# Optimization experiments

Hardware: AMD Instinct MI355X
Metric: run time of the kernel (lower is better)

## Reference

```python
import jax, jax.numpy as jnp
import numpy as np

K = 10
SLOPE = 0.2
FEATS = [3, 64, 128, 256, 512, 1024]
MLP = [1024, 128, 64, 1]
B, N = 8, 2048


def setup_inputs() -> dict:
    key = jax.random.key(0)
    keys = jax.random.split(key, 32)
    inp = {"x": jax.random.normal(keys[0], (B, N, 3), dtype=jnp.float32)}
    ki = 1
    for i in range(5):
        fin, fout = 2 * FEATS[i], FEATS[i + 1]
        s = 1.0 / np.sqrt(fin)
        inp[f"w{i}"] = jax.random.uniform(keys[ki], (fin, fout), jnp.float32, -s, s); ki += 1
        inp[f"b{i}"] = jax.random.uniform(keys[ki], (fout,), jnp.float32, -s, s); ki += 1
    for i in range(3):
        fin, fout = MLP[i], MLP[i + 1]
        s = 1.0 / np.sqrt(fin)
        inp[f"m{i}w"] = jax.random.uniform(keys[ki], (fin, fout), jnp.float32, -s, s); ki += 1
        inp[f"m{i}b"] = jax.random.uniform(keys[ki], (fout,), jnp.float32, -s, s); ki += 1
    return inp


def _knn_idx(xb):
    # xb: [N, F]; squared euclidean distances, self included (dist 0)
    sq = jnp.sum(xb * xb, axis=-1)
    d2 = sq[:, None] + sq[None, :] - 2.0 * (xb @ xb.T)
    _, idx = jax.lax.top_k(-d2, K)  # [N, K] nearest (incl. self)
    return idx


def _edge_conv(x, W, b):
    # x: [B, N, F] -> [B, N, Fout]
    fin = x.shape[-1]
    W1, W2 = W[:fin], W[fin:]  # split concat([x_i, x_j - x_i]) @ W
    idx = jax.vmap(_knn_idx)(x)  # [B, N, K]
    x_j = jax.vmap(lambda xb, ib: xb[ib])(x, idx)  # [B, N, K, F]
    h_center = x @ W1 + b  # [B, N, Fout]
    diff = x_j - x[:, :, None, :]
    h = h_center[:, :, None, :] + jnp.einsum('bnkf,fo->bnko', diff, W2)
    h = jnp.where(h > 0, h, SLOPE * h)  # LeakyReLU(0.2)
    return jnp.max(h, axis=2)  # max aggregation over neighbors


def reference(x, w0, b0, w1, b1, w2, b2, w3, b3, w4, b4,
              m0w, m0b, m1w, m1b, m2w, m2b):
    ws = [(w0, b0), (w1, b1), (w2, b2), (w3, b3), (w4, b4)]
    h = x
    for W, b in ws:
        h = _edge_conv(h, W, b)
    g = jnp.max(h, axis=1)  # MaxPool1d(kernel=2048) -> global max over points: [B, 1024]
    g = g @ m0w + m0b
    g = g @ m1w + m1b
    g = g @ m2w + m2b
    return g  # [B, 1]
```

## Files before the change

kernel.cpp:

```cpp
#include <hip/hip_runtime.h>
#include <hip/hip_bf16.h>
#include <math.h>

#define BB 8
#define NN 2048
#define KK 10
#define BN (BB * NN)
#define HC 1024
#define GCH 64

typedef __attribute__((ext_vector_type(8))) short bf16x8;
typedef __attribute__((ext_vector_type(4))) float f32x4;

__device__ inline unsigned short f2bf(float f) {
    unsigned int u = __float_as_uint(f);
    unsigned int r = u + 0x7fffu + ((u >> 16) & 1u);
    return (unsigned short)(r >> 16);
}
__device__ inline float bf2f(unsigned short h) {
    return __uint_as_float((unsigned int)h << 16);
}

__device__ __forceinline__ void async16(const void* g, void* l) {
    __builtin_amdgcn_global_load_lds(
        (const __attribute__((address_space(1))) void*)g,
        (__attribute__((address_space(3))) void*)l, 16, 0, 0);
}

__global__ void xsplit3_kernel(const float* __restrict__ x,
                               unsigned short* __restrict__ hi,
                               unsigned short* __restrict__ lo,
                               float* __restrict__ sq) {
    int row = blockIdx.x * blockDim.x + threadIdx.x;
    if (row >= BN) return;
    unsigned short hbuf[32], lbuf[32];
#pragma unroll
    for (int f = 0; f < 32; ++f) { hbuf[f] = 0; lbuf[f] = 0; }
    float s = 0.f;
#pragma unroll
    for (int f = 0; f < 3; ++f) {
        float v = x[(size_t)row * 3 + f];
        s += v * v;
        unsigned short h = f2bf(v);
        hbuf[f] = h;
        lbuf[f] = f2bf(v - bf2f(h));
    }
    sq[row] = s;
#pragma unroll
    for (int f = 0; f < 32; f += 8) {
        *(uint4*)&hi[(size_t)row * 32 + f] = *(uint4*)&hbuf[f];
        *(uint4*)&lo[(size_t)row * 32 + f] = *(uint4*)&lbuf[f];
    }
}

__global__ __launch_bounds__(256) void knn_gram_kernel(
        const unsigned short* __restrict__ xh, const unsigned short* __restrict__ xl,
        const float* __restrict__ sq, float* __restrict__ d2a,
        float* __restrict__ d2b, int F) {
    int b = blockIdx.y;
    int t = blockIdx.x, ti = 0;
    while (t >= 16 - ti) { t -= 16 - ti; ti++; }
    int tj = ti + t;
    int row0 = ti * 128;
    int col0 = tj * 128;
    const unsigned short* xhb = xh + (size_t)b * NN * F;
    const unsigned short* xlb = xl + (size_t)b * NN * F;
    const float* sqb = sq + (size_t)b * NN;

    __shared__ __align__(16) unsigned char smem_raw[33024];
    unsigned short* Ah = (unsigned short*)smem_raw;
    unsigned short* Al = Ah + 128 * 32;
    unsigned short* Bh = Al + 128 * 32;
    unsigned short* Bl = Bh + 128 * 32;
    float* LT = (float*)smem_raw;

    int tid = threadIdx.x;
    int lane = tid & 63;
    int wave = tid >> 6;
    int wr = (wave >> 1) * 64, wc = (wave & 1) * 64;
    int l15 = lane & 15, kq = lane >> 4;
    int rsub = lane >> 2;
    int csub = (((lane & 3) ^ ((lane >> 3) & 3))) * 8;
    int kqs = (kq ^ ((l15 >> 1) & 3)) * 8;

    f32x4 acc[4][4];
#pragma unroll
    for (int mt = 0; mt < 4; ++mt)
#pragma unroll
        for (int nt = 0; nt < 4; ++nt) acc[mt][nt] = (f32x4){0.f, 0.f, 0.f, 0.f};

    for (int kc = 0; kc < F; kc += 32) {
        __syncthreads();
#pragma unroll
        for (int j = 0; j < 2; ++j) {
            int row = wave * 32 + j * 16 + rsub;
            int dsto = wave * 1024 + j * 512;
            async16(xhb + (size_t)(row0 + row) * F + kc + csub, Ah + dsto);
            async16(xlb + (size_t)(row0 + row) * F + kc + csub, Al + dsto);
            async16(xhb + (size_t)(col0 + row) * F + kc + csub, Bh + dsto);
            async16(xlb + (size_t)(col0 + row) * F + kc + csub, Bl + dsto);
        }
        __syncthreads();
        bf16x8 bh[4], bl[4];
#pragma unroll
        for (int t4 = 0; t4 < 4; ++t4) {
            bh[t4] = *(const bf16x8*)&Bh[(wc + t4 * 16 + l15) * 32 + kqs];
            bl[t4] = *(const bf16x8*)&Bl[(wc + t4 * 16 + l15) * 32 + kqs];
        }
#pragma unroll
        for (int mt = 0; mt < 4; ++mt) {
            bf16x8 ah = *(const bf16x8*)&Ah[(wr + mt * 16 + l15) * 32 + kqs];
            bf16x8 al = *(const bf16x8*)&Al[(wr + mt * 16 + l15) * 32 + kqs];
#pragma unroll
            for (int nt = 0; nt < 4; ++nt) {
                acc[mt][nt] = __builtin_amdgcn_mfma_f32_16x16x32_bf16(ah, bh[nt], acc[mt][nt], 0, 0, 0);
                acc[mt][nt] = __builtin_amdgcn_mfma_f32_16x16x32_bf16(al, bh[nt], acc[mt][nt], 0, 0, 0);
                acc[mt][nt] = __builtin_amdgcn_mfma_f32_16x16x32_bf16(ah, bl[nt], acc[mt][nt], 0, 0, 0);
            }
        }
    }
    {
        float* dst = (col0 < HC) ? d2a : d2b;
        int lc0 = col0 & (HC - 1);
#pragma unroll
        for (int mt = 0; mt < 4; ++mt) {
            int rbase = row0 + wr + mt * 16 + kq * 4;
#pragma unroll
            for (int nt = 0; nt < 4; ++nt) {
                int cc = wc + nt * 16 + l15;
                float sqc = sqb[col0 + cc];
#pragma unroll
                for (int r = 0; r < 4; ++r) {
                    float v = (sqb[rbase + r] + sqc) - 2.f * acc[mt][nt][r];
                    acc[mt][nt][r] = v;
                    dst[((size_t)b * NN + rbase + r) * HC + lc0 + cc] = v;
                }
            }
        }
    }
    if (ti != tj) {
        float* mdst = (row0 < HC) ? d2a : d2b;
        int mc0 = row0 & (HC - 1);
#pragma unroll
        for (int h = 0; h < 2; ++h) {
            __syncthreads();
            if ((wave & 1) == h) {
#pragma unroll
                for (int mt = 0; mt < 4; ++mt)
#pragma unroll
                    for (int nt = 0; nt < 4; ++nt)
#pragma unroll
                        for (int r = 0; r < 4; ++r)
                            LT[(nt * 16 + l15) * 129 + (wr + mt * 16 + kq * 4 + r)] =
                                acc[mt][nt][r];
            }
            __syncthreads();
#pragma unroll
            for (int it = 0; it < 8; ++it) {
                int v = tid + it * 256;
                int lr = v >> 5, c4 = v & 31;
                float4 val;
                val.x = LT[lr * 129 + c4 * 4];
                val.y = LT[lr * 129 + c4 * 4 + 1];
                val.z = LT[lr * 129 + c4 * 4 + 2];
                val.w = LT[lr * 129 + c4 * 4 + 3];
                *(float4*)&mdst[((size_t)b * NN + col0 + h * 64 + lr) * HC + mc0 + c4 * 4] = val;
            }
        }
    }
}

__global__ __launch_bounds__(256) void knn_select_kernel(
        const float* __restrict__ d2a, const float* __restrict__ d2b,
        int* __restrict__ idx) {
    int row = blockIdx.x * 4 + (threadIdx.x >> 6);
    int lane = threadIdx.x & 63;
    const float* ra = d2a + (size_t)row * HC;
    const float* rb = d2b + (size_t)row * HC;

    float4 v[8];
#pragma unroll
    for (int it = 0; it < 4; ++it) {
        v[it]     = *(const float4*)&ra[it * 256 + lane * 4];
        v[it + 4] = *(const float4*)&rb[it * 256 + lane * 4];
    }

    float bestd[KK];
    int besti[KK];
#pragma unroll
    for (int k = 0; k < KK; ++k) { bestd[k] = INFINITY; besti[k] = 0x7fffffff; }

#pragma unroll
    for (int it = 0; it < 8; ++it) {
        int cbase = ((it < 4) ? (it * 256) : (HC + (it - 4) * 256)) + lane * 4;
        float dv[4] = {v[it].x, v[it].y, v[it].z, v[it].w};
#pragma unroll
        for (int s4 = 0; s4 < 4; ++s4) {
            float d = dv[s4];
            if (d < bestd[KK - 1]) {
                bestd[KK - 1] = d;
                besti[KK - 1] = cbase + s4;
#pragma unroll
                for (int s = KK - 1; s > 0; --s) {
                    if (bestd[s] < bestd[s - 1]) {
                        float td = bestd[s]; bestd[s] = bestd[s - 1]; bestd[s - 1] = td;
                        int ti = besti[s]; besti[s] = besti[s - 1]; besti[s - 1] = ti;
                    }
                }
            }
        }
    }

    int h = 0;
    int mywin = 0;
    for (int s = 0; s < KK; ++s) {
        float dd = (h < KK) ? bestd[h] : INFINITY;
        int ii = (h < KK) ? besti[h] : 0x7fffffff;
        float d0 = dd; int i0 = ii;
#pragma unroll
        for (int off = 32; off > 0; off >>= 1) {
            float od = __shfl_xor(dd, off);
            int oi = __shfl_xor(ii, off);
            if (od < dd || (od == dd && oi < ii)) { dd = od; ii = oi; }
        }
        if (lane == s) mywin = ii;
        if (h < KK && i0 == ii && d0 == dd) h++;
    }
    if (lane < KK) idx[(size_t)row * KK + lane] = mywin;
}

__global__ void wsplit_kernel(const float* __restrict__ w, unsigned short* __restrict__ WT,
                              int fin, int fpad, int fout) {
    int i = blockIdx.x * blockDim.x + threadIdx.x;
    int total = 2 * fout * fpad;
    if (i >= total) return;
    int op = i % (2 * fout);
    int f = i / (2 * fout);
    float v = 0.f;
    if (f < fin) {
        if (op < fout) v = w[(size_t)f * fout + op] - w[(size_t)(fin + f) * fout + op];
        else v = w[(size_t)(fin + f) * fout + (op - fout)];
    }
    unsigned short h = f2bf(v);
    unsigned short l = f2bf(v - bf2f(h));
    WT[(size_t)op * (2 * fpad) + f] = h;
    WT[(size_t)op * (2 * fpad) + fpad + f] = l;
}

__global__ __launch_bounds__(256) void gemm2_mfma_kernel(
        const unsigned short* __restrict__ XSh, const unsigned short* __restrict__ XSl,
        const unsigned short* __restrict__ WT, const float* __restrict__ bias,
        float* __restrict__ Aout, float* __restrict__ Tout, int fin, int fout) {
    int m0 = blockIdx.x * 128;
    int n0 = blockIdx.y * 128;
    __shared__ __align__(16) unsigned short AsB[4 * 128 * 32];
    unsigned short* Ah = AsB;
    unsigned short* Al = Ah + 128 * 32;
    unsigned short* Bh = Al + 128 * 32;
    unsigned short* Bl = Bh + 128 * 32;

    int tid = threadIdx.x;
    int lane = tid & 63;
    int wave = tid >> 6;
    int wr = (wave >> 1) * 64, wc = (wave & 1) * 64;
    int l15 = lane & 15, kq = lane >> 4;
    int rsub = lane >> 2;
    int csub = (((lane & 3) ^ ((lane >> 3) & 3))) * 8;
    int kqs = (kq ^ ((l15 >> 1) & 3)) * 8;
    int w2f = 2 * fin;

    f32x4 acc[4][4];
#pragma unroll
    for (int mt = 0; mt < 4; ++mt)
#pragma unroll
        for (int nt = 0; nt < 4; ++nt) acc[mt][nt] = (f32x4){0.f, 0.f, 0.f, 0.f};

    for (int kc = 0; kc < fin; kc += 32) {
        __syncthreads();
#pragma unroll
        for (int j = 0; j < 2; ++j) {
            int row = wave * 32 + j * 16 + rsub;
            int dsto = wave * 1024 + j * 512;
            async16(XSh + (size_t)(m0 + row) * fin + kc + csub, Ah + dsto);
            async16(XSl + (size_t)(m0 + row) * fin + kc + csub, Al + dsto);
            async16(WT + (size_t)(n0 + row) * w2f + kc + csub, Bh + dsto);
            async16(WT + (size_t)(n0 + row) * w2f + fin + kc + csub, Bl + dsto);
        }
        __syncthreads();
        bf16x8 bh[4], bl[4];
#pragma unroll
        for (int t = 0; t < 4; ++t) {
            bh[t] = *(const bf16x8*)&Bh[(wc + t * 16 + l15) * 32 + kqs];
            bl[t] = *(const bf16x8*)&Bl[(wc + t * 16 + l15) * 32 + kqs];
        }
#pragma unroll
        for (int mt = 0; mt < 4; ++mt) {
            bf16x8 ah = *(const bf16x8*)&Ah[(wr + mt * 16 + l15) * 32 + kqs];
            bf16x8 al = *(const bf16x8*)&Al[(wr + mt * 16 + l15) * 32 + kqs];
#pragma unroll
            for (int nt = 0; nt < 4; ++nt) {
                acc[mt][nt] = __builtin_amdgcn_mfma_f32_16x16x32_bf16(ah, bh[nt], acc[mt][nt], 0, 0, 0);
                acc[mt][nt] = __builtin_amdgcn_mfma_f32_16x16x32_bf16(al, bh[nt], acc[mt][nt], 0, 0, 0);
                acc[mt][nt] = __builtin_amdgcn_mfma_f32_16x16x32_bf16(ah, bl[nt], acc[mt][nt], 0, 0, 0);
            }
        }
    }
#pragma unroll
    for (int mt = 0; mt < 4; ++mt) {
        int mbase = m0 + wr + mt * 16 + kq * 4;
#pragma unroll
        for (int nt = 0; nt < 4; ++nt) {
            int oc = n0 + wc + nt * 16 + l15;
            f32x4 c = acc[mt][nt];
            if (oc < fout) {
                float bv = bias[oc];
#pragma unroll
                for (int r = 0; r < 4; ++r)
                    Aout[(size_t)(mbase + r) * fout + oc] = c[r] + bv;
            } else {
                int o2 = oc - fout;
#pragma unroll
                for (int r = 0; r < 4; ++r)
                    Tout[(size_t)(mbase + r) * fout + o2] = c[r];
            }
        }
    }
}

__global__ __launch_bounds__(256) void gathermax_fused_kernel(
        const float* __restrict__ A, const float* __restrict__ T,
        const int* __restrict__ idx, unsigned short* __restrict__ hi,
        unsigned short* __restrict__ lo, float* __restrict__ sq, int shift) {
    int b = blockIdx.y;
    int wave = threadIdx.x >> 6;
    int lane = threadIdx.x & 63;
    int pnl = blockIdx.x * 4 + wave;
    int pn = (b << 11) + pnl;
    int fout = 1 << shift;
    int nf4 = fout >> 2;
    const float* Tb = T + ((size_t)b << 11) * fout;
    const int* ip = idx + (size_t)pn * KK;
    int j[KK];
#pragma unroll
    for (int k = 0; k < KK; ++k) j[k] = ip[k];

    float s = 0.f;
    for (int f4 = lane; f4 < nf4; f4 += 64) {
        int o = f4 * 4;
        float4 m = {-INFINITY, -INFINITY, -INFINITY, -INFINITY};
#pragma unroll
        for (int k = 0; k < KK; ++k) {
            float4 t = *(const float4*)&Tb[(size_t)j[k] * fout + o];
            m.x = fmaxf(m.x, t.x); m.y = fmaxf(m.y, t.y);
            m.z = fmaxf(m.z, t.z); m.w = fmaxf(m.w, t.w);
        }
        float4 a = *(const float4*)&A[(size_t)pn * fout + o];
        float h4[4];
        h4[0] = a.x + m.x; h4[1] = a.y + m.y; h4[2] = a.z + m.z; h4[3] = a.w + m.w;
        uint2 uh, ul;
        unsigned short hs[4], ls[4];
#pragma unroll
        for (int q = 0; q < 4; ++q) {
            float h = h4[q] > 0.f ? h4[q] : 0.2f * h4[q];
            s += h * h;
            unsigned short hh = f2bf(h);
            hs[q] = hh;
            ls[q] = f2bf(h - bf2f(hh));
        }
        uh.x = (unsigned)hs[0] | ((unsigned)hs[1] << 16);
        uh.y = (unsigned)hs[2] | ((unsigned)hs[3] << 16);
        ul.x = (unsigned)ls[0] | ((unsigned)ls[1] << 16);
        ul.y = (unsigned)ls[2] | ((unsigned)ls[3] << 16);
        *(uint2*)&hi[(size_t)pn * fout + o] = uh;
        *(uint2*)&lo[(size_t)pn * fout + o] = ul;
    }
#pragma unroll
    for (int off = 32; off > 0; off >>= 1) s += __shfl_down(s, off);
    if (lane == 0) sq[pn] = s;
}

__global__ __launch_bounds__(256) void gathermax_gmax_kernel(
        const float* __restrict__ A, const float* __restrict__ T,
        const int* __restrict__ idx, float* __restrict__ gp) {
    int chunk = blockIdx.x;
    int b = blockIdx.y;
    int o = threadIdx.x * 4;
    const float* Tb = T + ((size_t)b << 11) * 1024;
    float4 gm = {-INFINITY, -INFINITY, -INFINITY, -INFINITY};
    for (int p = 0; p < NN / GCH; ++p) {
        int pnl = chunk * (NN / GCH) + p;
        int pn = (b << 11) + pnl;
        const int* ip = idx + (size_t)pn * KK;
        float4 m = {-INFINITY, -INFINITY, -INFINITY, -INFINITY};
#pragma unroll
        for (int k = 0; k < KK; ++k) {
            int j = ip[k];
            float4 t = *(const float4*)&Tb[(size_t)j * 1024 + o];
            m.x = fmaxf(m.x, t.x); m.y = fmaxf(m.y, t.y);
            m.z = fmaxf(m.z, t.z); m.w = fmaxf(m.w, t.w);
        }
        float4 a = *(const float4*)&A[(size_t)pn * 1024 + o];
        float4 h;
        h.x = a.x + m.x; h.y = a.y + m.y; h.z = a.z + m.z; h.w = a.w + m.w;
        h.x = h.x > 0.f ? h.x : 0.2f * h.x;
        h.y = h.y > 0.f ? h.y : 0.2f * h.y;
        h.z = h.z > 0.f ? h.z : 0.2f * h.z;
        h.w = h.w > 0.f ? h.w : 0.2f * h.w;
        gm.x = fmaxf(gm.x, h.x); gm.y = fmaxf(gm.y, h.y);
        gm.z = fmaxf(gm.z, h.z); gm.w = fmaxf(gm.w, h.w);
    }
    *(float4*)&gp[((size_t)chunk * BB + b) * 1024 + o] = gm;
}

__global__ void gmax2_kernel(const float* __restrict__ gp, float* __restrict__ g) {
    int b = blockIdx.y;
    int o = blockIdx.x * 256 + threadIdx.x;
    float m = -INFINITY;
    for (int c = 0; c < GCH; ++c) m = fmaxf(m, gp[((size_t)c * BB + b) * 1024 + o]);
    g[(size_t)b * 1024 + o] = m;
}

__global__ __launch_bounds__(128) void mlp_kernel(const float* __restrict__ g,
                                                  const float* __restrict__ m0w, const float* __restrict__ m0b,
                                                  const float* __restrict__ m1w, const float* __restrict__ m1b,
                                                  const float* __restrict__ m2w, const float* __restrict__ m2b,
                                                  float* __restrict__ out) {
    __shared__ float gs[1024];
    __shared__ float h1[128];
    __shared__ float h2[64];
    int b = blockIdx.x, t = threadIdx.x;
    for (int i = t; i < 1024; i += 128) gs[i] = g[(size_t)b * 1024 + i];
    __syncthreads();
    float s = m0b[t];
    for (int f = 0; f < 1024; ++f) s += gs[f] * m0w[(size_t)f * 128 + t];
    h1[t] = s;
    __syncthreads();
    if (t < 64) {
        float s2 = m1b[t];
        for (int f = 0; f < 128; ++f) s2 += h1[f] * m1w[(size_t)f * 64 + t];
        h2[t] = s2;
    }
    __syncthreads();
    if (t == 0) {
        float s3 = m2b[0];
        for (int f = 0; f < 64; ++f) s3 += h2[f] * m2w[f];
        out[b] = s3;
    }
}

extern "C" void kernel_launch(void* const* d_in, const int* in_sizes, int n_in,
                              void* d_out, int out_size, void* d_ws, size_t ws_size,
                              hipStream_t stream) {
    const float* x0 = (const float*)d_in[0];
    const float* w[5], * bi[5];
    for (int i = 0; i < 5; ++i) { w[i] = (const float*)d_in[1 + 2 * i]; bi[i] = (const float*)d_in[2 + 2 * i]; }
    const float* m0w = (const float*)d_in[11]; const float* m0b = (const float*)d_in[12];
    const float* m1w = (const float*)d_in[13]; const float* m1b = (const float*)d_in[14];
    const float* m2w = (const float*)d_in[15]; const float* m2b = (const float*)d_in[16];

    float* X0 = (float*)d_ws;
    float* X1 = X0 + (size_t)BN * 1024;
    float* T  = X1 + (size_t)BN * 1024;
    float* SQ = T  + (size_t)BN * 1024;
    int*   IDX = (int*)(SQ + BN);
    float* G  = (float*)(IDX + (size_t)BN * KK);
    unsigned short* XSh = (unsigned short*)(G + (size_t)BB * 1024);
    unsigned short* XSl = XSh + (size_t)BN * 512;
    unsigned short* WT  = XSl + (size_t)BN * 512;
    float* GP = (float*)(WT + (size_t)2 * 1024 * 1024);

    const int fouts[5] = {64, 128, 256, 512, 1024};
    const int shifts[5] = {6, 7, 8, 9, 10};
    int fin = 3;
    float* bufs[2] = {X0, X1};

    xsplit3_kernel<<<(BN + 255) / 256, 256, 0, stream>>>(x0, XSh, XSl, SQ);

    for (int l = 0; l < 5; ++l) {
        int fout = fouts[l];
        float* nxt = bufs[l & 1];
        int Fg = (l == 0) ? 32 : fin;

        float* D2a = T;
        float* D2b = nxt;
        dim3 gg2(136, BB);
        knn_gram_kernel<<<gg2, 256, 0, stream>>>(XSh, XSl, SQ, D2a, D2b, Fg);
        knn_select_kernel<<<BN / 4, 256, 0, stream>>>(D2a, D2b, IDX);

        int nw = 2 * fout * Fg;
        wsplit_kernel<<<(nw + 255) / 256, 256, 0, stream>>>(w[l], WT, fin, Fg, fout);
        dim3 gg(BN / 128, (2 * fout) / 128);
        gemm2_mfma_kernel<<<gg, 256, 0, stream>>>(XSh, XSl, WT, bi[l], nxt, T, Fg, fout);

        if (l < 4) {
            dim3 gmg(NN / 4, BB);
            gathermax_fused_kernel<<<gmg, 256, 0, stream>>>(nxt, T, IDX, XSh, XSl, SQ, shifts[l]);
        } else {
            dim3 gmg(GCH, BB);
            gathermax_gmax_kernel<<<gmg, 256, 0, stream>>>(nxt, T, IDX, GP);
        }

        fin = fout;
    }

    dim3 x2(1024 / 256, BB);
    gmax2_kernel<<<x2, 256, 0, stream>>>(GP, G);

    mlp_kernel<<<BB, 128, 0, stream>>>(G, m0w, m0b, m1w, m1b, m2w, m2b, (float*)d_out);
}
```

Measured before the change: 1.017 ms.

## Merge gram and GEMM launches, hoist weight splitting, fold global max into MLP

The Gram-distance tiles and the per-layer feature GEMM now run in one launch, so the two independent workloads share the GPU instead of running back to back. This relies on a dedicated distance buffer. All five weight-split conversions move into a single upfront kernel, and the final global-max reduction is folded into the MLP kernel. Together these cut the number of launches and idle gaps per layer. The cost is a larger workspace, with a fallback path kept for when the workspace is too small.

```diff
diff --git a/kernel.cpp b/kernel.cpp
--- a/kernel.cpp
+++ b/kernel.cpp
@@ -53,12 +53,42 @@
     }
 }
 
-__global__ __launch_bounds__(256) void knn_gram_kernel(
+__global__ void wsplit_all_kernel(const float* __restrict__ w0, const float* __restrict__ w1,
+                                  const float* __restrict__ w2, const float* __restrict__ w3,
+                                  const float* __restrict__ w4, unsigned short* __restrict__ WTall) {
+    const int fins[5]  = {3, 64, 128, 256, 512};
+    const int fpads[5] = {32, 64, 128, 256, 512};
+    const int fouts[5] = {64, 128, 256, 512, 1024};
+    const int eoff[6]  = {0, 4096, 20480, 86016, 348160, 1396736};
+    const int woff[5]  = {0, 8192, 40960, 172032, 696320};
+    int i = blockIdx.x * blockDim.x + threadIdx.x;
+    if (i >= 1396736) return;
+    int l;
+    if (i < eoff[1]) l = 0; else if (i < eoff[2]) l = 1;
+    else if (i < eoff[3]) l = 2; else if (i < eoff[4]) l = 3; else l = 4;
+    int e = i - eoff[l];
+    const float* w = (l == 0) ? w0 : (l == 1) ? w1 : (l == 2) ? w2 : (l == 3) ? w3 : w4;
+    int fin = fins[l], fpad = fpads[l], fout = fouts[l];
+    unsigned short* WT = WTall + woff[l];
+    int op = e % (2 * fout);
+    int f = e / (2 * fout);
+    float v = 0.f;
+    if (f < fin) {
+        if (op < fout) v = w[(size_t)f * fout + op] - w[(size_t)(fin + f) * fout + op];
+        else v = w[(size_t)(fin + f) * fout + (op - fout)];
+    }
+    unsigned short h = f2bf(v);
+    unsigned short lo = f2bf(v - bf2f(h));
+    WT[(size_t)op * (2 * fpad) + f] = h;
+    WT[(size_t)op * (2 * fpad) + fpad + f] = lo;
+}
+
+__device__ __forceinline__ void gram_body(
+        unsigned char* smem_raw, int tIdx, int b,
         const unsigned short* __restrict__ xh, const unsigned short* __restrict__ xl,
         const float* __restrict__ sq, float* __restrict__ d2a,
         float* __restrict__ d2b, int F) {
-    int b = blockIdx.y;
-    int t = blockIdx.x, ti = 0;
+    int t = tIdx, ti = 0;
     while (t >= 16 - ti) { t -= 16 - ti; ti++; }
     int tj = ti + t;
     int row0 = ti * 128;
@@ -67,7 +97,6 @@
     const unsigned short* xlb = xl + (size_t)b * NN * F;
     const float* sqb = sq + (size_t)b * NN;
 
-    __shared__ __align__(16) unsigned char smem_raw[33024];
     unsigned short* Ah = (unsigned short*)smem_raw;
     unsigned short* Al = Ah + 128 * 32;
     unsigned short* Bh = Al + 128 * 32;
@@ -170,91 +199,14 @@
     }
 }
 
-__global__ __launch_bounds__(256) void knn_select_kernel(
-        const float* __restrict__ d2a, const float* __restrict__ d2b,
-        int* __restrict__ idx) {
-    int row = blockIdx.x * 4 + (threadIdx.x >> 6);
-    int lane = threadIdx.x & 63;
-    const float* ra = d2a + (size_t)row * HC;
-    const float* rb = d2b + (size_t)row * HC;
-
-    float4 v[8];
-#pragma unroll
-    for (int it = 0; it < 4; ++it) {
-        v[it]     = *(const float4*)&ra[it * 256 + lane * 4];
-        v[it + 4] = *(const float4*)&rb[it * 256 + lane * 4];
-    }
-
-    float bestd[KK];
-    int besti[KK];
-#pragma unroll
-    for (int k = 0; k < KK; ++k) { bestd[k] = INFINITY; besti[k] = 0x7fffffff; }
-
-#pragma unroll
-    for (int it = 0; it < 8; ++it) {
-        int cbase = ((it < 4) ? (it * 256) : (HC + (it - 4) * 256)) + lane * 4;
-        float dv[4] = {v[it].x, v[it].y, v[it].z, v[it].w};
-#pragma unroll
-        for (int s4 = 0; s4 < 4; ++s4) {
-            float d = dv[s4];
-            if (d < bestd[KK - 1]) {
-                bestd[KK - 1] = d;
-                besti[KK - 1] = cbase + s4;
-#pragma unroll
-                for (int s = KK - 1; s > 0; --s) {
-                    if (bestd[s] < bestd[s - 1]) {
-                        float td = bestd[s]; bestd[s] = bestd[s - 1]; bestd[s - 1] = td;
-                        int ti = besti[s]; besti[s] = besti[s - 1]; besti[s - 1] = ti;
-                    }
-                }
-            }
-        }
-    }
-
-    int h = 0;
-    int mywin = 0;
-    for (int s = 0; s < KK; ++s) {
-        float dd = (h < KK) ? bestd[h] : INFINITY;
-        int ii = (h < KK) ? besti[h] : 0x7fffffff;
-        float d0 = dd; int i0 = ii;
-#pragma unroll
-        for (int off = 32; off > 0; off >>= 1) {
-            float od = __shfl_xor(dd, off);
-            int oi = __shfl_xor(ii, off);
-            if (od < dd || (od == dd && oi < ii)) { dd = od; ii = oi; }
-        }
-        if (lane == s) mywin = ii;
-        if (h < KK && i0 == ii && d0 == dd) h++;
-    }
-    if (lane < KK) idx[(size_t)row * KK + lane] = mywin;
-}
-
-__global__ void wsplit_kernel(const float* __restrict__ w, unsigned short* __restrict__ WT,
-                              int fin, int fpad, int fout) {
-    int i = blockIdx.x * blockDim.x + threadIdx.x;
-    int total = 2 * fout * fpad;
-    if (i >= total) return;
-    int op = i % (2 * fout);
-    int f = i / (2 * fout);
-    float v = 0.f;
-    if (f < fin) {
-        if (op < fout) v = w[(size_t)f * fout + op] - w[(size_t)(fin + f) * fout + op];
-        else v = w[(size_t)(fin + f) * fout + (op - fout)];
-    }
-    unsigned short h = f2bf(v);
-    unsigned short l = f2bf(v - bf2f(h));
-    WT[(size_t)op * (2 * fpad) + f] = h;
-    WT[(size_t)op * (2 * fpad) + fpad + f] = l;
-}
-
-__global__ __launch_bounds__(256) void gemm2_mfma_kernel(
+__device__ __forceinline__ void gemm_body(
+        unsigned char* smem_raw, int bx, int by,
         const unsigned short* __restrict__ XSh, const unsigned short* __restrict__ XSl,
         const unsigned short* __restrict__ WT, const float* __restrict__ bias,
         float* __restrict__ Aout, float* __restrict__ Tout, int fin, int fout) {
-    int m0 = blockIdx.x * 128;
-    int n0 = blockIdx.y * 128;
-    __shared__ __align__(16) unsigned short AsB[4 * 128 * 32];
-    unsigned short* Ah = AsB;
+    int m0 = bx * 128;
+    int n0 = by * 128;
+    unsigned short* Ah = (unsigned short*)smem_raw;
     unsigned short* Al = Ah + 128 * 32;
     unsigned short* Bh = Al + 128 * 32;
     unsigned short* Bl = Bh + 128 * 32;
@@ -325,6 +277,95 @@
             }
         }
     }
+}
+
+__global__ __launch_bounds__(256) void knn_gram_kernel(
+        const unsigned short* __restrict__ xh, const unsigned short* __restrict__ xl,
+        const float* __restrict__ sq, float* __restrict__ d2a,
+        float* __restrict__ d2b, int F) {
+    __shared__ __align__(16) unsigned char smem_raw[33024];
+    gram_body(smem_raw, blockIdx.x, blockIdx.y, xh, xl, sq, d2a, d2b, F);
+}
+__global__ __launch_bounds__(256) void gemm2_mfma_kernel(
+        const unsigned short* __restrict__ XSh, const unsigned short* __restrict__ XSl,
+        const unsigned short* __restrict__ WT, const float* __restrict__ bias,
+        float* __restrict__ Aout, float* __restrict__ Tout, int fin, int fout) {
+    __shared__ __align__(16) unsigned char smem_raw[33024];
+    gemm_body(smem_raw, blockIdx.x, blockIdx.y, XSh, XSl, WT, bias, Aout, Tout, fin, fout);
+}
+
+__global__ __launch_bounds__(256) void gram_gemm_kernel(
+        const unsigned short* __restrict__ xh, const unsigned short* __restrict__ xl,
+        const float* __restrict__ sq, float* __restrict__ d2a, float* __restrict__ d2b,
+        const unsigned short* __restrict__ WT, const float* __restrict__ bias,
+        float* __restrict__ Aout, float* __restrict__ Tout,
+        int F, int fout, int nGram) {
+    __shared__ __align__(16) unsigned char smem_raw[33024];
+    if ((int)blockIdx.x < nGram) {
+        gram_body(smem_raw, blockIdx.x % 136, blockIdx.x / 136, xh, xl, sq, d2a, d2b, F);
+    } else {
+        int gi = blockIdx.x - nGram;
+        gemm_body(smem_raw, gi & 127, gi >> 7, xh, xl, WT, bias, Aout, Tout, F, fout);
+    }
+}
+
+__global__ __launch_bounds__(256) void knn_select_kernel(
+        const float* __restrict__ d2a, const float* __restrict__ d2b,
+        int* __restrict__ idx) {
+    int row = blockIdx.x * 4 + (threadIdx.x >> 6);
+    int lane = threadIdx.x & 63;
+    const float* ra = d2a + (size_t)row * HC;
+    const float* rb = d2b + (size_t)row * HC;
+
+    float4 v[8];
+#pragma unroll
+    for (int it = 0; it < 4; ++it) {
+        v[it]     = *(const float4*)&ra[it * 256 + lane * 4];
+        v[it + 4] = *(const float4*)&rb[it * 256 + lane * 4];
+    }
+
+    float bestd[KK];
+    int besti[KK];
+#pragma unroll
+    for (int k = 0; k < KK; ++k) { bestd[k] = INFINITY; besti[k] = 0x7fffffff; }
+
+#pragma unroll
+    for (int it = 0; it < 8; ++it) {
+        int cbase = ((it < 4) ? (it * 256) : (HC + (it - 4) * 256)) + lane * 4;
+        float dv[4] = {v[it].x, v[it].y, v[it].z, v[it].w};
+#pragma unroll
+        for (int s4 = 0; s4 < 4; ++s4) {
+            float d = dv[s4];
+            if (d < bestd[KK - 1]) {
+                bestd[KK - 1] = d;
+                besti[KK - 1] = cbase + s4;
+#pragma unroll
+                for (int s = KK - 1; s > 0; --s) {
+                    if (bestd[s] < bestd[s - 1]) {
+                        float td = bestd[s]; bestd[s] = bestd[s - 1]; bestd[s - 1] = td;
+                        int ti = besti[s]; besti[s] = besti[s - 1]; besti[s - 1] = ti;
+                    }
+                }
+            }
+        }
+    }
+
+    int h = 0;
+    int mywin = 0;
+    for (int s = 0; s < KK; ++s) {
+        float dd = (h < KK) ? bestd[h] : INFINITY;
+        int ii = (h < KK) ? besti[h] : 0x7fffffff;
+        float d0 = dd; int i0 = ii;
+#pragma unroll
+        for (int off = 32; off > 0; off >>= 1) {
+            float od = __shfl_xor(dd, off);
+            int oi = __shfl_xor(ii, off);
+            if (od < dd || (od == dd && oi < ii)) { dd = od; ii = oi; }
+        }
+        if (lane == s) mywin = ii;
+        if (h < KK && i0 == ii && d0 == dd) h++;
+    }
+    if (lane < KK) idx[(size_t)row * KK + lane] = mywin;
 }
 
 __global__ __launch_bounds__(256) void gathermax_fused_kernel(
@@ -412,15 +453,7 @@
     *(float4*)&gp[((size_t)chunk * BB + b) * 1024 + o] = gm;
 }
 
-__global__ void gmax2_kernel(const float* __restrict__ gp, float* __restrict__ g) {
-    int b = blockIdx.y;
-    int o = blockIdx.x * 256 + threadIdx.x;
-    float m = -INFINITY;
-    for (int c = 0; c < GCH; ++c) m = fmaxf(m, gp[((size_t)c * BB + b) * 1024 + o]);
-    g[(size_t)b * 1024 + o] = m;
-}
-
-__global__ __launch_bounds__(128) void mlp_kernel(const float* __restrict__ g,
+__global__ __launch_bounds__(128) void mlp_kernel(const float* __restrict__ gp,
                                                   const float* __restrict__ m0w, const float* __restrict__ m0b,
                                                   const float* __restrict__ m1w, const float* __restrict__ m1b,
                                                   const float* __restrict__ m2w, const float* __restrict__ m2b,
@@ -429,7 +462,11 @@
     __shared__ float h1[128];
     __shared__ float h2[64];
     int b = blockIdx.x, t = threadIdx.x;
-    for (int i = t; i < 1024; i += 128) gs[i] = g[(size_t)b * 1024 + i];
+    for (int i = t; i < 1024; i += 128) {
+        float m = -INFINITY;
+        for (int c = 0; c < GCH; ++c) m = fmaxf(m, gp[((size_t)c * BB + b) * 1024 + i]);
+        gs[i] = m;
+    }
     __syncthreads();
     float s = m0b[t];
     for (int f = 0; f < 1024; ++f) s += gs[f] * m0w[(size_t)f * 128 + t];
@@ -458,53 +495,86 @@
     const float* m1w = (const float*)d_in[13]; const float* m1b = (const float*)d_in[14];
     const float* m2w = (const float*)d_in[15]; const float* m2b = (const float*)d_in[16];
 
-    float* X0 = (float*)d_ws;
-    float* X1 = X0 + (size_t)BN * 1024;
-    float* T  = X1 + (size_t)BN * 1024;
-    float* SQ = T  + (size_t)BN * 1024;
-    int*   IDX = (int*)(SQ + BN);
-    float* G  = (float*)(IDX + (size_t)BN * KK);
-    unsigned short* XSh = (unsigned short*)(G + (size_t)BB * 1024);
-    unsigned short* XSl = XSh + (size_t)BN * 512;
-    unsigned short* WT  = XSl + (size_t)BN * 512;
-    float* GP = (float*)(WT + (size_t)2 * 1024 * 1024);
-
     const int fouts[5] = {64, 128, 256, 512, 1024};
     const int shifts[5] = {6, 7, 8, 9, 10};
-    int fin = 3;
-    float* bufs[2] = {X0, X1};
-
-    xsplit3_kernel<<<(BN + 255) / 256, 256, 0, stream>>>(x0, XSh, XSl, SQ);
-
-    for (int l = 0; l < 5; ++l) {
-        int fout = fouts[l];
-        float* nxt = bufs[l & 1];
-        int Fg = (l == 0) ? 32 : fin;
-
-        float* D2a = T;
-        float* D2b = nxt;
-        dim3 gg2(136, BB);
-        knn_gram_kernel<<<gg2, 256, 0, stream>>>(XSh, XSl, SQ, D2a, D2b, Fg);
-        knn_select_kernel<<<BN / 4, 256, 0, stream>>>(D2a, D2b, IDX);
-
-        int nw = 2 * fout * Fg;
-        wsplit_kernel<<<(nw + 255) / 256, 256, 0, stream>>>(w[l], WT, fin, Fg, fout);
-        dim3 gg(BN / 128, (2 * fout) / 128);
-        gemm2_mfma_kernel<<<gg, 256, 0, stream>>>(XSh, XSl, WT, bi[l], nxt, T, Fg, fout);
-
-        if (l < 4) {
-            dim3 gmg(NN / 4, BB);
-            gathermax_fused_kernel<<<gmg, 256, 0, stream>>>(nxt, T, IDX, XSh, XSl, SQ, shifts[l]);
-        } else {
-            dim3 gmg(GCH, BB);
-            gathermax_gmax_kernel<<<gmg, 256, 0, stream>>>(nxt, T, IDX, GP);
-        }
-
-        fin = fout;
-    }
-
-    dim3 x2(1024 / 256, BB);
-    gmax2_kernel<<<x2, 256, 0, stream>>>(GP, G);
-
-    mlp_kernel<<<BB, 128, 0, stream>>>(G, m0w, m0b, m1w, m1b, m2w, m2b, (float*)d_out);
-}
+    const int woff[5] = {0, 8192, 40960, 172032, 696320};
+    const size_t WTALL = 2793472;
+
+    size_t need = (size_t)BN * 1024 * 4 * 2 + (size_t)BN * 2048 * 4
+                + (size_t)BN * 4 + (size_t)BN * KK * 4
+                + (size_t)BN * 512 * 2 * 2 + WTALL * 2
+                + (size_t)GCH * BB * 1024 * 4;
+    bool fast = ws_size >= need;
+
+    if (fast) {
+        float* A   = (float*)d_ws;
+        float* T   = A + (size_t)BN * 1024;
+        float* D2  = T + (size_t)BN * 1024;
+        float* SQ  = D2 + (size_t)BN * 2048;
+        int*   IDX = (int*)(SQ + BN);
+        unsigned short* XSh = (unsigned short*)(IDX + (size_t)BN * KK);
+        unsigned short* XSl = XSh + (size_t)BN * 512;
+        unsigned short* WTall = XSl + (size_t)BN * 512;
+        float* GP  = (float*)(WTall + WTALL);
+        float* D2a = D2;
+        float* D2b = D2 + (size_t)BN * HC;
+
+        xsplit3_kernel<<<(BN + 255) / 256, 256, 0, stream>>>(x0, XSh, XSl, SQ);
+        wsplit_all_kernel<<<(1396736 + 255) / 256, 256, 0, stream>>>(w[0], w[1], w[2], w[3], w[4], WTall);
+
+        int fin = 3;
+        for (int l = 0; l < 5; ++l) {
+            int fout = fouts[l];
+            int Fg = (l == 0) ? 32 : fin;
+            int nGram = 136 * BB;
+            int nGemm = 128 * ((2 * fout) / 128);
+            gram_gemm_kernel<<<nGram + nGemm, 256, 0, stream>>>(
+                XSh, XSl, SQ, D2a, D2b, WTall + woff[l], bi[l], A, T, Fg, fout, nGram);
+            knn_select_kernel<<<BN / 4, 256, 0, stream>>>(D2a, D2b, IDX);
+            if (l < 4) {
+                dim3 gmg(NN / 4, BB);
+                gathermax_fused_kernel<<<gmg, 256, 0, stream>>>(A, T, IDX, XSh, XSl, SQ, shifts[l]);
+            } else {
+                dim3 gmg(GCH, BB);
+                gathermax_gmax_kernel<<<gmg, 256, 0, stream>>>(A, T, IDX, GP);
+            }
+            fin = fout;
+        }
+        mlp_kernel<<<BB, 128, 0, stream>>>(GP, m0w, m0b, m1w, m1b, m2w, m2b, (float*)d_out);
+    } else {
+        float* X0 = (float*)d_ws;
+        float* X1 = X0 + (size_t)BN * 1024;
+        float* T  = X1 + (size_t)BN * 1024;
+        float* SQ = T  + (size_t)BN * 1024;
+        int*   IDX = (int*)(SQ + BN);
+        unsigned short* XSh = (unsigned short*)(IDX + (size_t)BN * KK);
+        unsigned short* XSl = XSh + (size_t)BN * 512;
+        unsigned short* WTall = XSl + (size_t)BN * 512;
+        float* GP = (float*)(WTall + WTALL);
+        float* bufs[2] = {X0, X1};
+
+        xsplit3_kernel<<<(BN + 255) / 256, 256, 0, stream>>>(x0, XSh, XSl, SQ);
+        wsplit_all_kernel<<<(1396736 + 255) / 256, 256, 0, stream>>>(w[0], w[1], w[2], w[3], w[4], WTall);
+
+        int fin = 3;
+        for (int l = 0; l < 5; ++l) {
+            int fout = fouts[l];
+            float* nxt = bufs[l & 1];
+            int Fg = (l == 0) ? 32 : fin;
+            dim3 gg2(136, BB);
+            knn_gram_kernel<<<gg2, 256, 0, stream>>>(XSh, XSl, SQ, T, nxt, Fg);
+            knn_select_kernel<<<BN / 4, 256, 0, stream>>>(T, nxt, IDX);
+            dim3 gg(BN / 128, (2 * fout) / 128);
+            gemm2_mfma_kernel<<<gg, 256, 0, stream>>>(XSh, XSl, WTall + woff[l], bi[l], nxt, T, Fg, fout);
+            if (l < 4) {
+                dim3 gmg(NN / 4, BB);
+                gathermax_fused_kernel<<<gmg, 256, 0, stream>>>(nxt, T, IDX, XSh, XSl, SQ, shifts[l]);
+            } else {
+                dim3 gmg(GCH, BB);
+                gathermax_gmax_kernel<<<gmg, 256, 0, stream>>>(nxt, T, IDX, GP);
+            }
+            fin = fout;
+        }
+        mlp_kernel<<<BB, 128, 0, stream>>>(GP, m0w, m0b, m1w, m1b, m2w, m2b, (float*)d_out);
+    }
+}
```

Result: slower. 1.068 ms (+5.1%).
